# Kernel optimization log

Hardware: AMD Instinct MI355X
Metric: run time of the kernel (lower is better)

## Reference

```python
import jax, jax.numpy as jnp
import numpy as np


def _conv1x1(x, w, b=None):
    # x: [B,C,H,W], w: [O,C]
    y = jnp.einsum('bchw,oc->bohw', x, w)
    if b is not None:
        y = y + b[None, :, None, None]
    return y


def _conv3x3_dilated(x, w, b, dil):
    p = dil  # padding == dilation keeps spatial size for 3x3 kernels
    y = jax.lax.conv_general_dilated(
        x, w, window_strides=(1, 1), padding=((p, p), (p, p)),
        rhs_dilation=(dil, dil), dimension_numbers=('NCHW', 'OIHW', 'NCHW'))
    return y + b[None, :, None, None]


def _upsample2x_align_corners(x):
    # bilinear, align_corners=True, scale factor 2
    B, C, H, W = x.shape
    oh, ow = 2 * H, 2 * W
    ys = jnp.linspace(0.0, H - 1.0, oh)
    xs = jnp.linspace(0.0, W - 1.0, ow)
    y0 = jnp.floor(ys).astype(jnp.int32)
    x0 = jnp.floor(xs).astype(jnp.int32)
    y1 = jnp.minimum(y0 + 1, H - 1)
    x1 = jnp.minimum(x0 + 1, W - 1)
    wy = (ys - y0)[None, None, :, None]
    wx = (xs - x0)[None, None, None, :]
    gt = x[:, :, y0, :]
    gb = x[:, :, y1, :]
    top = gt[:, :, :, x0] * (1 - wx) + gt[:, :, :, x1] * wx
    bot = gb[:, :, :, x0] * (1 - wx) + gb[:, :, :, x1] * wx
    return top * (1 - wy) + bot * wy


def _gr(ftr, ck_w, ck_b, avg_w, max_w, gcn_w):
    # GR module: attention-diagonal graph conv with degree normalization
    B, C, H, W = ftr.shape
    HW = H * W
    # ChannelAttention_diag -> diagonal entries cw: [B, M]
    avg = ftr.mean(axis=(2, 3))
    mx = ftr.max(axis=(2, 3))
    cw = jax.nn.sigmoid(jax.nn.relu(avg @ avg_w.T) + jax.nn.relu(mx @ max_w.T))  # [B,M]
    k = jax.nn.relu(_conv1x1(ftr, ck_w, ck_b)).reshape(B, -1, HW)  # [B,M,HW]
    q = jnp.swapaxes(k, 1, 2)  # [B,HW,M]
    # A = sigmoid(q @ diag(cw) @ k); degree d = rowsum(A)^(-1/2)
    A = jax.nn.sigmoid(jnp.einsum('bim,bm,bmj->bij', q, cw, k))  # [B,HW,HW]
    d = A.sum(axis=2) ** -0.5  # [B,HW]
    P = d[:, :, None] * q  # D^{-1/2} @ q, [B,HW,M]
    X = jnp.swapaxes(ftr.reshape(B, C, HW), 1, 2)  # [B,HW,C]
    PtX = jnp.einsum('bjm,bjc->bmc', P, X)  # [B,M,C]
    LX = X - jnp.einsum('bim,bmc->bic', P, cw[:, :, None] * PtX)
    Y = X + LX @ gcn_w  # GCN (no bias)
    return jnp.swapaxes(Y, 1, 2).reshape(B, C, H, W)


def setup_inputs() -> dict:
    key = jax.random.key(0)
    ks = jax.random.split(key, 20)
    B, C = 64, 1024
    Cq = C // 4  # 256
    Mi = Cq // 2  # 128, ChannelAttention inter channels
    s = 0.02
    inp = {
        'x_cur': jax.random.normal(ks[0], (B, C, 16, 16), jnp.float32),
        'x_lat': jax.random.normal(ks[1], (B, C, 8, 8), jnp.float32),
        'conv_w': jax.random.normal(ks[2], (Cq, C), jnp.float32) * s,
        'conv_b': jax.random.normal(ks[3], (Cq,), jnp.float32) * s,
        'conv1_w': jax.random.normal(ks[4], (C, Cq), jnp.float32) * s,
        'conv1_b': jax.random.normal(ks[5], (C,), jnp.float32) * s,
        'conv3_w': jax.random.normal(ks[6], (C, 3 * Cq), jnp.float32) * s,
        'conv3_b': jax.random.normal(ks[7], (C,), jnp.float32) * s,
        'rate0_w': jax.random.normal(ks[8], (Cq, C, 3, 3), jnp.float32) * s,
        'rate0_b': jax.random.normal(ks[9], (Cq,), jnp.float32) * s,
        'rate1_w': jax.random.normal(ks[10], (Cq, C, 3, 3), jnp.float32) * s,
        'rate1_b': jax.random.normal(ks[11], (Cq,), jnp.float32) * s,
        'rate2_w': jax.random.normal(ks[12], (Cq, C, 3, 3), jnp.float32) * s,
        'rate2_b': jax.random.normal(ks[13], (Cq,), jnp.float32) * s,
        'gr_ck_w': jax.random.normal(ks[14], (Mi, Cq), jnp.float32) * s,
        'gr_ck_b': jax.random.normal(ks[15], (Mi,), jnp.float32) * s,
        'gr_avg_w': jax.random.normal(ks[16], (Mi, Cq), jnp.float32) * s,
        'gr_max_w': jax.random.normal(ks[17], (Mi, Cq), jnp.float32) * s,
        'gr_gcn_w': jax.random.normal(ks[18], (Cq, Cq), jnp.float32) * s,
        'pre': 1,
    }
    return inp


def reference(x_cur, x_lat, conv_w, conv_b, conv1_w, conv1_b, conv3_w, conv3_b,
              rate0_w, rate0_b, rate1_w, rate1_b, rate2_w, rate2_b,
              gr_ck_w, gr_ck_b, gr_avg_w, gr_max_w, gr_gcn_w, pre):
    # pre == 1 path of Graph_aspp.forward
    gr_args = (gr_ck_w, gr_ck_b, gr_avg_w, gr_max_w, gr_gcn_w)
    x_sum = x_cur * _upsample2x_align_corners(x_lat) + x_cur
    f1 = _conv3x3_dilated(x_sum, rate0_w, rate0_b, 1) + _conv1x1(x_sum, conv_w, conv_b)
    x1 = _gr(f1, *gr_args)
    feature = _conv1x1(f1, conv1_w, conv1_b) + x_sum
    f2 = _conv3x3_dilated(feature, rate1_w, rate1_b, 2) + _conv1x1(feature, conv_w, conv_b)
    x2 = _gr(f2, *gr_args)
    feature = _conv1x1(f2, conv1_w, conv1_b) + x_sum
    f3 = _conv3x3_dilated(feature, rate2_w, rate2_b, 4) + _conv1x1(feature, conv_w, conv_b)
    x3 = _gr(f3, *gr_args)
    cat = jnp.concatenate((x1, x2, x3), axis=1)
    return _conv1x1(cat, conv3_w, conv3_b)
```

## Files before the change

kernel.cpp:

```cpp
#include <hip/hip_runtime.h>

typedef unsigned short ushort_t;
typedef unsigned int uint32;
typedef __attribute__((ext_vector_type(8))) unsigned short ushort8;
typedef __attribute__((ext_vector_type(8))) __bf16 bf16x8;
typedef __attribute__((ext_vector_type(4))) float f32x4;

__device__ __forceinline__ ushort_t f2b(float f) {
    union { float f; uint32 u; } v; v.f = f;
    uint32 r = v.u + 0x7fffu + ((v.u >> 16) & 1u);
    return (ushort_t)(r >> 16);
}
__device__ __forceinline__ float b2f(ushort_t b) {
    union { uint32 u; float f; } v; v.u = ((uint32)b) << 16;
    return v.f;
}
__device__ __forceinline__ float sigm(float x) { return 1.f / (1.f + __expf(-x)); }

__device__ __forceinline__ void gload_lds16(const void* g, void* l) {
    __builtin_amdgcn_global_load_lds(
        (__attribute__((address_space(1))) void*)g,
        (__attribute__((address_space(3))) void*)l, 16, 0, 0);
}

constexpr int EPI_RELU  = 1;
constexpr int EPI_FEAT  = 2;
constexpr int EPI_SIG   = 3;
constexpr int EPI_XG    = 4;
constexpr int EPI_NEGCW = 5;
constexpr int EPI_Y     = 6;
constexpr int EPI_OUTT  = 7;

struct GemmP {
    const ushort_t* A; const ushort_t* B;
    const ushort_t* A2; const ushort_t* B2;
    long long aBatch, bBatch, a2Batch, b2Batch;
    int lda, ldb, lda2, ldb2;
    int Ksub, kSplit, dil;
    const float* bias;
    const ushort_t* res; long long resBatch; int ldres;
    ushort_t* obf; long long oBatch; int ldo;
    ushort_t* obf2;
    float* of32;
    const float* cw;
    float* dsum;
    const ushort_t* zpage;
};

__global__ __launch_bounds__(256) void gemm_big(GemmP p) {
    __shared__ __align__(16) ushort_t aT[128 * 64];
    __shared__ __align__(16) ushort_t bT[128 * 64];
    const int tid = threadIdx.x;
    const int z = blockIdx.z;
    const int m0 = blockIdx.x * 128, n0 = blockIdx.y * 128;
    const int lane = tid & 63, wid = tid >> 6;
    const int l15 = lane & 15, l16 = lane >> 4;
    const int wr = wid >> 1, wc = wid & 1;
    const int lrow = lane >> 3;
    const int sgran = (lane & 7) ^ lrow;

    int ayy[4], axx[4];
    const ushort_t* aBase[4];
    const ushort_t* bBase[4];
#pragma unroll
    for (int i = 0; i < 4; ++i) {
        int row = wid * 32 + i * 8 + lrow;
        int m = m0 + row;
        int bb = m >> 8;
        ayy[i] = (m >> 4) & 15; axx[i] = m & 15;
        aBase[i] = p.A + (long long)bb * 262144 + sgran * 8;
        bBase[i] = p.B + (long long)(n0 + row) * p.ldb + sgran * 8;
    }

    f32x4 acc[4][4];
#pragma unroll
    for (int i = 0; i < 4; ++i)
#pragma unroll
        for (int j = 0; j < 4; ++j) acc[i][j] = (f32x4){0.f, 0.f, 0.f, 0.f};

    const int gk0 = z * p.kSplit;
    const int iters = p.Ksub >> 6;
    for (int it = 0; it < iters; ++it) {
        const int gk = gk0 + it * 64;
        const int tap = gk >> 10, kin = gk & 1023;
        int dy = 0, dx = 0;
        if (tap < 9) { int ky = tap / 3; dy = (ky - 1) * p.dil; dx = (tap - ky * 3 - 1) * p.dil; }
#pragma unroll
        for (int i = 0; i < 4; ++i) {
            int iy = ayy[i] + dy, ix = axx[i] + dx;
            bool ok = ((unsigned)iy < 16u) && ((unsigned)ix < 16u);
            const ushort_t* ga = ok ? (aBase[i] + (((iy << 4) + ix) << 10) + kin) : p.zpage;
            gload_lds16(ga, &aT[(wid * 32 + i * 8) * 64]);
        }
#pragma unroll
        for (int i = 0; i < 4; ++i)
            gload_lds16(bBase[i] + gk, &bT[(wid * 32 + i * 8) * 64]);
        asm volatile("s_waitcnt vmcnt(0)" ::: "memory");
        __syncthreads();
#pragma unroll
        for (int ks = 0; ks < 2; ++ks) {
            bf16x8 af[4], bfr[4];
#pragma unroll
            for (int mi = 0; mi < 4; ++mi) {
                int rr = wr * 64 + mi * 16 + l15;
                int cc = (ks * 32 + l16 * 8) ^ ((rr & 7) << 3);
                af[mi] = __builtin_bit_cast(bf16x8, *(const ushort8*)&aT[rr * 64 + cc]);
            }
#pragma unroll
            for (int ni = 0; ni < 4; ++ni) {
                int rr = wc * 64 + ni * 16 + l15;
                int cc = (ks * 32 + l16 * 8) ^ ((rr & 7) << 3);
                bfr[ni] = __builtin_bit_cast(bf16x8, *(const ushort8*)&bT[rr * 64 + cc]);
            }
#pragma unroll
            for (int mi = 0; mi < 4; ++mi)
#pragma unroll
                for (int ni = 0; ni < 4; ++ni)
                    acc[mi][ni] = __builtin_amdgcn_mfma_f32_16x16x32_bf16(af[mi], bfr[ni], acc[mi][ni], 0, 0, 0);
        }
        __syncthreads();
    }
#pragma unroll
    for (int mi = 0; mi < 4; ++mi)
#pragma unroll
        for (int ni = 0; ni < 4; ++ni) {
            int gcol = n0 + wc * 64 + ni * 16 + l15;
            int growb = m0 + wr * 64 + mi * 16 + l16 * 4;
#pragma unroll
            for (int r = 0; r < 4; ++r)
                p.obf[(long long)z * p.oBatch + (long long)(growb + r) * 256 + gcol] =
                    f2b(acc[mi][ni][r]);
        }
}

template<int BM, int BN, int AMODE, int EPI>
__global__ __launch_bounds__(256) void gemm_k(GemmP p) {
    __shared__ __align__(16) ushort_t aT[BM * 64];
    __shared__ __align__(16) ushort_t bT[BN * 64];
    constexpr int APASS = BM / 32, BPASS = BN / 32;
    constexpr int MFRAG = BM / 32, NFRAG = BN / 32;
    const int tid = threadIdx.x;
    const int z = blockIdx.z;
    const int m0 = blockIdx.x * BM, n0 = blockIdx.y * BN;
    const int lane = tid & 63, wid = tid >> 6;
    const int l15 = lane & 15, l16 = lane >> 4;
    const int wr = wid >> 1, wc = wid & 1;
    const int srow = tid >> 3, scol = (tid & 7) * 8;
    const int swcol = scol ^ ((srow & 7) << 3);

    const ushort_t* aptr[APASS];
    const ushort_t* bptr[BPASS];
    const ushort_t* aptr2[APASS];
    const ushort_t* bptr2[BPASS];
#pragma unroll
    for (int pi = 0; pi < APASS; ++pi)
        aptr[pi] = p.A + (long long)z * p.aBatch +
                   (long long)(m0 + pi * 32 + srow) * p.lda + scol;
#pragma unroll
    for (int pi = 0; pi < BPASS; ++pi)
        bptr[pi] = p.B + (long long)z * p.bBatch +
                   (long long)(n0 + pi * 32 + srow) * p.ldb + scol;
    if constexpr (AMODE == 2) {
#pragma unroll
        for (int pi = 0; pi < APASS; ++pi)
            aptr2[pi] = p.A2 + (long long)z * p.a2Batch +
                        (long long)(m0 + pi * 32 + srow) * p.lda2 + scol;
#pragma unroll
        for (int pi = 0; pi < BPASS; ++pi)
            bptr2[pi] = p.B2 + (long long)z * p.b2Batch +
                        (long long)(n0 + pi * 32 + srow) * p.ldb2 + scol;
    }

    f32x4 acc[MFRAG][NFRAG];
#pragma unroll
    for (int i = 0; i < MFRAG; ++i)
#pragma unroll
        for (int j = 0; j < NFRAG; ++j) acc[i][j] = (f32x4){0.f, 0.f, 0.f, 0.f};

    ushort8 ar[APASS], br[BPASS];
    auto ldg = [&](int gk) {
        if (AMODE == 2 && gk >= 256) {
            int g2 = gk - 256;
#pragma unroll
            for (int pi = 0; pi < APASS; ++pi) ar[pi] = *(const ushort8*)(aptr2[pi] + g2);
#pragma unroll
            for (int pi = 0; pi < BPASS; ++pi) br[pi] = *(const ushort8*)(bptr2[pi] + g2);
        } else {
#pragma unroll
            for (int pi = 0; pi < APASS; ++pi) ar[pi] = *(const ushort8*)(aptr[pi] + gk);
#pragma unroll
            for (int pi = 0; pi < BPASS; ++pi) br[pi] = *(const ushort8*)(bptr[pi] + gk);
        }
    };

    const int gk0 = z * p.kSplit;
    ldg(gk0);
    const int iters = p.Ksub >> 6;
    for (int it = 0; it < iters; ++it) {
#pragma unroll
        for (int pi = 0; pi < APASS; ++pi)
            *(ushort8*)&aT[(pi * 32 + srow) * 64 + swcol] = ar[pi];
#pragma unroll
        for (int pi = 0; pi < BPASS; ++pi)
            *(ushort8*)&bT[(pi * 32 + srow) * 64 + swcol] = br[pi];
        __syncthreads();
        if (it + 1 < iters) ldg(gk0 + (it + 1) * 64);
#pragma unroll
        for (int ks = 0; ks < 2; ++ks) {
            bf16x8 af[MFRAG], bfr[NFRAG];
#pragma unroll
            for (int mi = 0; mi < MFRAG; ++mi) {
                int rr = wr * (BM / 2) + mi * 16 + l15;
                int cc = (ks * 32 + l16 * 8) ^ ((rr & 7) << 3);
                af[mi] = __builtin_bit_cast(bf16x8, *(const ushort8*)&aT[rr * 64 + cc]);
            }
#pragma unroll
            for (int ni = 0; ni < NFRAG; ++ni) {
                int rr = wc * (BN / 2) + ni * 16 + l15;
                int cc = (ks * 32 + l16 * 8) ^ ((rr & 7) << 3);
                bfr[ni] = __builtin_bit_cast(bf16x8, *(const ushort8*)&bT[rr * 64 + cc]);
            }
#pragma unroll
            for (int mi = 0; mi < MFRAG; ++mi)
#pragma unroll
                for (int ni = 0; ni < NFRAG; ++ni)
                    acc[mi][ni] = __builtin_amdgcn_mfma_f32_16x16x32_bf16(af[mi], bfr[ni], acc[mi][ni], 0, 0, 0);
        }
        __syncthreads();
    }

#pragma unroll
    for (int mi = 0; mi < MFRAG; ++mi) {
        if constexpr (EPI == EPI_SIG) {
#pragma unroll
            for (int r = 0; r < 4; ++r) {
                float sv = 0.f;
#pragma unroll
                for (int ni = 0; ni < NFRAG; ++ni) sv += sigm(acc[mi][ni][r]);
                sv += __shfl_xor(sv, 1); sv += __shfl_xor(sv, 2);
                sv += __shfl_xor(sv, 4); sv += __shfl_xor(sv, 8);
                if (l15 == 0) {
                    int grow = m0 + wr * (BM / 2) + mi * 16 + l16 * 4 + r;
                    int q4 = blockIdx.y * 2 + wc;
                    p.dsum[q4 * 16384 + z * 256 + grow] = sv;
                }
            }
        } else {
#pragma unroll
            for (int ni = 0; ni < NFRAG; ++ni) {
                int gcol = n0 + wc * (BN / 2) + ni * 16 + l15;
                int growb = m0 + wr * (BM / 2) + mi * 16 + l16 * 4;
#pragma unroll
                for (int r = 0; r < 4; ++r) {
                    int grow = growb + r;
                    float v = acc[mi][ni][r];
                    if constexpr (EPI == EPI_RELU) {
                        v += p.bias[gcol]; v = fmaxf(v, 0.f);
                        p.obf[(long long)grow * p.ldo + gcol] = f2b(v);
                        p.obf2[(long long)grow * p.ldo + gcol] =
                            f2b(v * p.cw[((grow >> 8) << 7) + gcol]);
                    } else if constexpr (EPI == EPI_FEAT) {
                        v += p.bias[gcol] + b2f(p.res[(long long)grow * p.ldres + gcol]);
                        p.obf[(long long)grow * p.ldo + gcol] = f2b(v);
                    } else if constexpr (EPI == EPI_XG) {
                        p.obf[(long long)z * p.oBatch + (long long)grow * p.ldo + gcol] = f2b(v);
                    } else if constexpr (EPI == EPI_NEGCW) {
                        v *= -p.cw[z * 128 + gcol];
                        p.obf[(long long)z * p.oBatch + (long long)grow * p.ldo + gcol] = f2b(v);
                    } else if constexpr (EPI == EPI_Y) {
                        v = b2f(p.res[(long long)z * p.resBatch + (long long)grow * p.ldres + gcol]) + v;
                        p.obf[(long long)z * p.oBatch + (long long)grow * p.ldo + gcol] = f2b(v);
                    } else if constexpr (EPI == EPI_OUTT) {
                        v += p.bias[grow];
                        int bb = gcol >> 8, px = gcol & 255;
                        p.of32[((long long)bb * 1024 + grow) * 256 + px] = v;
                    }
                }
            }
        }
    }
}


__global__ void k_combine(const ushort_t* __restrict__ t, const float* __restrict__ fbias_s,
                          ushort_t* __restrict__ f) {
    int idx = blockIdx.x * 256 + threadIdx.x;
    const long long N = 16384ll * 256;
    ushort8 a0 = *(const ushort8*)(t + (long long)idx * 8);
    ushort8 a1 = *(const ushort8*)(t + N + (long long)idx * 8);
    ushort8 a2 = *(const ushort8*)(t + 2 * N + (long long)idx * 8);
    ushort8 a3 = *(const ushort8*)(t + 3 * N + (long long)idx * 8);
    ushort8 a4 = *(const ushort8*)(t + 4 * N + (long long)idx * 8);
    int cb = (idx * 8) & 255;
    ushort8 o;
#pragma unroll
    for (int k = 0; k < 8; ++k)
        o[k] = f2b(b2f(a0[k]) + b2f(a1[k]) + b2f(a2[k]) + b2f(a3[k]) + b2f(a4[k]) + fbias_s[cb + k]);
    *(ushort8*)&f[(long long)idx * 8] = o;
}

__global__ void k_upsum(const float* __restrict__ xc, const float* __restrict__ xl,
                        ushort_t* __restrict__ xs) {
    __shared__ float lat[64 * 64];
    __shared__ ushort_t tile[64 * 258];
    int b = blockIdx.x, c0 = blockIdx.y * 64;
    int t = threadIdx.x;
    for (int i = t; i < 4096; i += 256)
        lat[i] = xl[((long long)(b * 1024 + c0 + (i >> 6))) * 64 + (i & 63)];
    __syncthreads();
    int y = t >> 4, x = t & 15;
    float fy = y * (7.f / 15.f); int y0 = (int)fy; float wy = fy - y0; int y1 = y0 + 1 > 7 ? 7 : y0 + 1;
    float fx = x * (7.f / 15.f); int x0 = (int)fx; float wx = fx - x0; int x1 = x0 + 1 > 7 ? 7 : x0 + 1;
    for (int cc = 0; cc < 64; ++cc) {
        float cur = xc[((long long)(b * 1024 + c0 + cc)) * 256 + t];
        const float* L = &lat[cc * 64];
        float tv = L[y0 * 8 + x0] * (1.f - wx) + L[y0 * 8 + x1] * wx;
        float bv = L[y1 * 8 + x0] * (1.f - wx) + L[y1 * 8 + x1] * wx;
        float up = tv + (bv - tv) * wy;
        tile[cc * 258 + t] = f2b(cur * (1.f + up));
    }
    __syncthreads();
    for (int i = t; i < 16384; i += 256) {
        int px = i >> 6, cc = i & 63;
        xs[((long long)(b * 256 + px)) * 1024 + c0 + cc] = tile[cc * 258 + px];
    }
}

__global__ void k_poolcw(const ushort_t* __restrict__ f,
                         const float* __restrict__ aw, const float* __restrict__ mw,
                         float* __restrict__ cw) {
    __shared__ float sa[256], sm[256];
    int b = blockIdx.x, t = threadIdx.x;
    float s = 0.f, m = -3.4e38f;
    const ushort_t* base = f + (long long)b * 65536 + t;
    for (int px = 0; px < 256; ++px) { float v = b2f(base[px * 256]); s += v; m = fmaxf(m, v); }
    sa[t] = s * (1.f / 256.f);
    sm[t] = m;
    __syncthreads();
    if (t < 128) {
        float s1 = 0.f, s2 = 0.f;
        const float* a = aw + t * 256; const float* w = mw + t * 256;
        for (int c = 0; c < 256; ++c) { s1 += sa[c] * a[c]; s2 += sm[c] * w[c]; }
        s1 = fmaxf(s1, 0.f); s2 = fmaxf(s2, 0.f);
        cw[b * 128 + t] = sigm(s1 + s2);
    }
}

__global__ void k_pscale(const ushort_t* __restrict__ q, const float* __restrict__ dsum4,
                         ushort_t* __restrict__ P, ushort_t* __restrict__ Pt) {
    __shared__ ushort_t t[128][130];
    __shared__ float dd[128];
    int jh = blockIdx.x, b = blockIdx.y;
    int j0 = jh * 128;
    int tid = threadIdx.x;
    if (tid < 128) {
        int pix = b * 256 + j0 + tid;
        float s = dsum4[pix] + dsum4[16384 + pix] + dsum4[32768 + pix] + dsum4[49152 + pix];
        dd[tid] = rsqrtf(s);
    }
    __syncthreads();
    int jr = tid >> 7, m = tid & 127;
    for (int i = 0; i < 64; ++i) {
        int j = i * 2 + jr;
        long long qi = ((long long)(b * 256 + j0 + j)) * 128 + m;
        ushort_t v = f2b(dd[j] * b2f(q[qi]));
        P[qi] = v;
        t[j][m] = v;
    }
    __syncthreads();
    for (int i = 0; i < 64; ++i) {
        int mm = i * 2 + jr;
        Pt[((long long)b << 15) + (mm << 8) + j0 + m] = t[m][mm];
    }
}

__global__ void k_packall(const float* r0, const float* r1, const float* r2,
                          const float* convw, const float* c1w, const float* c3w,
                          const float* ckw, const float* gcnw,
                          const float* rb0, const float* rb1, const float* rb2,
                          const float* cb,
                          ushort_t* wbig3, ushort_t* w1b, ushort_t* w3b,
                          ushort_t* ckb, ushort_t* gcnT, float* fbias,
                          ushort_t* zpage) {
    int blk = blockIdx.x, tid = threadIdx.x;
    if (blk < 768) {
        __shared__ float lw[10240];
        int s = blk >> 8, o = blk & 255;
        const float* rate = s == 0 ? r0 : (s == 1 ? r1 : r2);
        for (int i = tid; i < 9216; i += 256) lw[i] = rate[(long long)o * 9216 + i];
        for (int i = tid; i < 1024; i += 256) lw[9216 + i] = convw[(long long)o * 1024 + i];
        __syncthreads();
        ushort_t* dst = wbig3 + (long long)blk * 10240;
        for (int i = tid; i < 10240; i += 256) {
            int tap = i >> 10, ci = i & 1023;
            float v = (tap < 9) ? lw[ci * 9 + tap] : lw[9216 + i - 9216 + ci - ci];
            v = (tap < 9) ? lw[ci * 9 + tap] : lw[9216 + ci];
            dst[i] = f2b(v);
        }
        return;
    }
    const int R1 = 262144, R2 = R1 + 786432, R3 = R2 + 32768, R4 = R3 + 65536;
    const int R5 = R4 + 768, R6 = R5 + 128;
    int base = (blk - 768) * 2048 + tid * 8;
#pragma unroll
    for (int k = 0; k < 8; ++k) {
        int i = base + k;
        if (i >= R6) return;
        if (i < R1) w1b[i] = f2b(c1w[i]);
        else if (i < R2) w3b[i - R1] = f2b(c3w[i - R1]);
        else if (i < R3) ckb[i - R2] = f2b(ckw[i - R2]);
        else if (i < R4) {
            int ii = i - R3; int c2 = ii >> 8, c1 = ii & 255;
            gcnT[ii] = f2b(gcnw[c1 * 256 + c2]);
        } else if (i < R5) {
            int ii = i - R4; int s = ii >> 8, t = ii & 255;
            const float* rb = s == 0 ? rb0 : (s == 1 ? rb1 : rb2);
            fbias[ii] = rb[t] + cb[t];
        } else {
            zpage[i - R5] = 0;
        }
    }
}

__global__ void k_sentinel(float* o, int n, float v) {
    int i = blockIdx.x * 256 + threadIdx.x; if (i < n) o[i] = v;
}

extern "C" void kernel_launch(void* const* d_in, const int* in_sizes, int n_in,
                              void* d_out, int out_size, void* d_ws, size_t ws_size,
                              hipStream_t stream) {
    const float* x_cur  = (const float*)d_in[0];
    const float* x_lat  = (const float*)d_in[1];
    const float* conv_w = (const float*)d_in[2];
    const float* conv_b = (const float*)d_in[3];
    const float* conv1_w = (const float*)d_in[4];
    const float* conv1_b = (const float*)d_in[5];
    const float* conv3_w = (const float*)d_in[6];
    const float* conv3_b = (const float*)d_in[7];
    const float* rate_w[3] = {(const float*)d_in[8], (const float*)d_in[10], (const float*)d_in[12]};
    const float* rate_b[3] = {(const float*)d_in[9], (const float*)d_in[11], (const float*)d_in[13]};
    const float* ck_w  = (const float*)d_in[14];
    const float* ck_b  = (const float*)d_in[15];
    const float* avg_w = (const float*)d_in[16];
    const float* max_w = (const float*)d_in[17];
    const float* gcn_w = (const float*)d_in[18];
    float* out = (float*)d_out;

    char* w = (char*)d_ws;
    auto take = [&](size_t bytes) { void* p = (void*)w; w += (bytes + 255) & ~(size_t)255; return p; };
    ushort_t* xsum  = (ushort_t*)take(16384ll * 1024 * 2);
    ushort_t* feat  = (ushort_t*)take(16384ll * 1024 * 2);
    ushort_t* fbuf  = (ushort_t*)take(16384ll * 256 * 2);
    ushort_t* xgt   = (ushort_t*)take(64ll * 256 * 256 * 2);
    ushort_t* qbuf  = (ushort_t*)take(16384ll * 128 * 2);
    ushort_t* qc    = (ushort_t*)take(16384ll * 128 * 2);
    ushort_t* Pt    = (ushort_t*)take(64ll * 128 * 256 * 2);
    ushort_t* Pb    = (ushort_t*)take(16384ll * 128 * 2);
    ushort_t* Htn   = (ushort_t*)take(64ll * 256 * 128 * 2);
    ushort_t* wbig3 = (ushort_t*)take(3ll * 256 * 10240 * 2);
    ushort_t* w1b   = (ushort_t*)take(1024ll * 256 * 2);
    ushort_t* w3b   = (ushort_t*)take(1024ll * 768 * 2);
    ushort_t* ckb   = (ushort_t*)take(128ll * 256 * 2);
    ushort_t* gcnT  = (ushort_t*)take(256ll * 256 * 2);
    ushort_t* zpage = (ushort_t*)take(256);
    float*    fbias = (float*)take(3 * 256 * 4);
    float*    cwb   = (float*)take(64 * 128 * 4);
    float*    dsum4 = (float*)take(4ll * 64 * 256 * 4);
    ushort_t* catb  = (ushort_t*)take(16384ll * 768 * 2);
    ushort_t* ftmp  = (ushort_t*)take(5ll * 16384 * 256 * 2);
    size_t need = (size_t)(w - (char*)d_ws);

    if (need > ws_size) {
        float v = 1.0e6f + (float)(ws_size >> 20);
        k_sentinel<<<(out_size + 255) / 256, 256, 0, stream>>>(out, out_size, v);
        return;
    }

    k_packall<<<768 + 561, 256, 0, stream>>>(
        rate_w[0], rate_w[1], rate_w[2], conv_w, conv1_w, conv3_w, ck_w, gcn_w,
        rate_b[0], rate_b[1], rate_b[2], conv_b,
        wbig3, w1b, w3b, ckb, gcnT, fbias, zpage);
    k_upsum<<<dim3(64, 16), 256, 0, stream>>>(x_cur, x_lat, xsum);

    for (int s = 0; s < 3; ++s) {
        {
            GemmP p{};
            p.A = (s == 0) ? xsum : feat;
            p.B = wbig3 + (long long)s * 256 * 10240; p.ldb = 10240;
            p.Ksub = 2048; p.kSplit = 2048; p.dil = 1 << s;
            p.obf = ftmp; p.oBatch = 16384ll * 256;
            p.zpage = zpage;
            gemm_big<<<dim3(128, 2, 5), 256, 0, stream>>>(p);
        }
        k_combine<<<2048, 256, 0, stream>>>(ftmp, fbias + s * 256, fbuf);
        k_poolcw<<<64, 256, 0, stream>>>(fbuf, avg_w, max_w, cwb);
        {
            GemmP p{};
            p.A = fbuf; p.lda = 256; p.B = ckb; p.ldb = 256;
            p.Ksub = 256;
            p.bias = ck_b; p.obf = qbuf; p.obf2 = qc; p.cw = cwb; p.ldo = 128;
            gemm_k<128, 128, 0, EPI_RELU><<<dim3(128, 1, 1), 256, 0, stream>>>(p);
        }
        {
            GemmP p{};
            p.A = qc;   p.aBatch = 32768; p.lda = 128;
            p.B = qbuf; p.bBatch = 32768; p.ldb = 128;
            p.Ksub = 128; p.dsum = dsum4;
            gemm_k<128, 128, 0, EPI_SIG><<<dim3(2, 2, 64), 256, 0, stream>>>(p);
        }
        k_pscale<<<dim3(2, 64), 256, 0, stream>>>(qbuf, dsum4, Pb, Pt);
        {
            GemmP p{};
            p.A = gcnT; p.aBatch = 0;     p.lda = 256;
            p.B = fbuf; p.bBatch = 65536; p.ldb = 256;
            p.Ksub = 256;
            p.obf = xgt; p.oBatch = 65536; p.ldo = 256;
            gemm_k<128, 128, 0, EPI_XG><<<dim3(2, 2, 64), 256, 0, stream>>>(p);
        }
        {
            GemmP p{};
            p.A = xgt; p.aBatch = 65536; p.lda = 256;
            p.B = Pt;  p.bBatch = 32768; p.ldb = 256;
            p.Ksub = 256; p.cw = cwb;
            p.obf = Htn; p.oBatch = 32768; p.ldo = 128;
            gemm_k<128, 128, 0, EPI_NEGCW><<<dim3(2, 1, 64), 256, 0, stream>>>(p);
        }
        {
            GemmP p{};
            p.A = fbuf; p.aBatch = 65536; p.lda = 256;
            p.B = gcnT; p.bBatch = 0;     p.ldb = 256;
            p.A2 = Pb;  p.a2Batch = 32768; p.lda2 = 128;
            p.B2 = Htn; p.b2Batch = 32768; p.ldb2 = 128;
            p.Ksub = 384;
            p.res = fbuf; p.resBatch = 65536; p.ldres = 256;
            p.obf = catb + s * 256; p.oBatch = 256ll * 768; p.ldo = 768;
            gemm_k<128, 128, 2, EPI_Y><<<dim3(2, 2, 64), 256, 0, stream>>>(p);
        }
        if (s < 2) {
            GemmP p{};
            p.A = fbuf; p.lda = 256; p.B = w1b; p.ldb = 256;
            p.Ksub = 256; p.bias = conv1_b;
            p.res = xsum; p.ldres = 1024;
            p.obf = feat; p.ldo = 1024;
            gemm_k<128, 128, 0, EPI_FEAT><<<dim3(128, 8, 1), 256, 0, stream>>>(p);
        }
    }
    {
        GemmP p{};
        p.A = w3b;  p.lda = 768;
        p.B = catb; p.ldb = 768;
        p.Ksub = 768; p.bias = conv3_b; p.of32 = out;
        gemm_k<128, 128, 0, EPI_OUTT><<<dim3(8, 128, 1), 256, 0, stream>>>(p);
    }
}
```

Baseline: 762.1 us.

## Use 64x64 tiles for small GR GEMMs and fold cw scaling into A-load

Switches the graph-reasoning GEMMs (ck conv, attention/sigmoid degree sum, XG, NEGCW, Y, conv1 feature) from 128x128 to 64x64 tiles with proportionally larger grids, so these small batched GEMMs launch more blocks and fill more compute units. The cw-scaled copy of q is no longer written by the ReLU epilogue. Instead a new A-load mode multiplies A by cw while loading, which removes one buffer write and read. The degree partial sums grow from 4 to 8 slices to match the finer column split. The tradeoff is less operand reuse per tile and an extra multiply-and-round on every A element load.

```diff
diff --git a/kernel.cpp b/kernel.cpp
--- a/kernel.cpp
+++ b/kernel.cpp
@@ -40,7 +40,6 @@
     const float* bias;
     const ushort_t* res; long long resBatch; int ldres;
     ushort_t* obf; long long oBatch; int ldo;
-    ushort_t* obf2;
     float* of32;
     const float* cw;
     float* dsum;
@@ -185,6 +184,17 @@
             for (int pi = 0; pi < APASS; ++pi) ar[pi] = *(const ushort8*)(aptr2[pi] + g2);
 #pragma unroll
             for (int pi = 0; pi < BPASS; ++pi) br[pi] = *(const ushort8*)(bptr2[pi] + g2);
+        } else if constexpr (AMODE == 3) {
+#pragma unroll
+            for (int pi = 0; pi < APASS; ++pi) {
+                ushort8 t8 = *(const ushort8*)(aptr[pi] + gk);
+#pragma unroll
+                for (int k = 0; k < 8; ++k)
+                    t8[k] = f2b(b2f(t8[k]) * p.cw[(z << 7) + gk + scol + k]);
+                ar[pi] = t8;
+            }
+#pragma unroll
+            for (int pi = 0; pi < BPASS; ++pi) br[pi] = *(const ushort8*)(bptr[pi] + gk);
         } else {
 #pragma unroll
             for (int pi = 0; pi < APASS; ++pi) ar[pi] = *(const ushort8*)(aptr[pi] + gk);
@@ -241,8 +251,8 @@
                 sv += __shfl_xor(sv, 4); sv += __shfl_xor(sv, 8);
                 if (l15 == 0) {
                     int grow = m0 + wr * (BM / 2) + mi * 16 + l16 * 4 + r;
-                    int q4 = blockIdx.y * 2 + wc;
-                    p.dsum[q4 * 16384 + z * 256 + grow] = sv;
+                    int q8 = blockIdx.y * 2 + wc;
+                    p.dsum[q8 * 16384 + z * 256 + grow] = sv;
                 }
             }
         } else {
@@ -257,8 +267,6 @@
                     if constexpr (EPI == EPI_RELU) {
                         v += p.bias[gcol]; v = fmaxf(v, 0.f);
                         p.obf[(long long)grow * p.ldo + gcol] = f2b(v);
-                        p.obf2[(long long)grow * p.ldo + gcol] =
-                            f2b(v * p.cw[((grow >> 8) << 7) + gcol]);
                     } else if constexpr (EPI == EPI_FEAT) {
                         v += p.bias[gcol] + b2f(p.res[(long long)grow * p.ldres + gcol]);
                         p.obf[(long long)grow * p.ldo + gcol] = f2b(v);
@@ -346,7 +354,7 @@
     }
 }
 
-__global__ void k_pscale(const ushort_t* __restrict__ q, const float* __restrict__ dsum4,
+__global__ void k_pscale(const ushort_t* __restrict__ q, const float* __restrict__ dsum8,
                          ushort_t* __restrict__ P, ushort_t* __restrict__ Pt) {
     __shared__ ushort_t t[128][130];
     __shared__ float dd[128];
@@ -355,7 +363,9 @@
     int tid = threadIdx.x;
     if (tid < 128) {
         int pix = b * 256 + j0 + tid;
-        float s = dsum4[pix] + dsum4[16384 + pix] + dsum4[32768 + pix] + dsum4[49152 + pix];
+        float s = 0.f;
+#pragma unroll
+        for (int qs = 0; qs < 8; ++qs) s += dsum8[qs * 16384 + pix];
         dd[tid] = rsqrtf(s);
     }
     __syncthreads();
@@ -393,8 +403,7 @@
         ushort_t* dst = wbig3 + (long long)blk * 10240;
         for (int i = tid; i < 10240; i += 256) {
             int tap = i >> 10, ci = i & 1023;
-            float v = (tap < 9) ? lw[ci * 9 + tap] : lw[9216 + i - 9216 + ci - ci];
-            v = (tap < 9) ? lw[ci * 9 + tap] : lw[9216 + ci];
+            float v = (tap < 9) ? lw[ci * 9 + tap] : lw[9216 + ci];
             dst[i] = f2b(v);
         }
         return;
@@ -453,7 +462,6 @@
     ushort_t* fbuf  = (ushort_t*)take(16384ll * 256 * 2);
     ushort_t* xgt   = (ushort_t*)take(64ll * 256 * 256 * 2);
     ushort_t* qbuf  = (ushort_t*)take(16384ll * 128 * 2);
-    ushort_t* qc    = (ushort_t*)take(16384ll * 128 * 2);
     ushort_t* Pt    = (ushort_t*)take(64ll * 128 * 256 * 2);
     ushort_t* Pb    = (ushort_t*)take(16384ll * 128 * 2);
     ushort_t* Htn   = (ushort_t*)take(64ll * 256 * 128 * 2);
@@ -465,7 +473,7 @@
     ushort_t* zpage = (ushort_t*)take(256);
     float*    fbias = (float*)take(3 * 256 * 4);
     float*    cwb   = (float*)take(64 * 128 * 4);
-    float*    dsum4 = (float*)take(4ll * 64 * 256 * 4);
+    float*    dsum8 = (float*)take(8ll * 64 * 256 * 4);
     ushort_t* catb  = (ushort_t*)take(16384ll * 768 * 2);
     ushort_t* ftmp  = (ushort_t*)take(5ll * 16384 * 256 * 2);
     size_t need = (size_t)(w - (char*)d_ws);
@@ -498,24 +506,24 @@
             GemmP p{};
             p.A = fbuf; p.lda = 256; p.B = ckb; p.ldb = 256;
             p.Ksub = 256;
-            p.bias = ck_b; p.obf = qbuf; p.obf2 = qc; p.cw = cwb; p.ldo = 128;
-            gemm_k<128, 128, 0, EPI_RELU><<<dim3(128, 1, 1), 256, 0, stream>>>(p);
+            p.bias = ck_b; p.obf = qbuf; p.ldo = 128;
+            gemm_k<64, 64, 0, EPI_RELU><<<dim3(256, 2, 1), 256, 0, stream>>>(p);
         }
         {
             GemmP p{};
-            p.A = qc;   p.aBatch = 32768; p.lda = 128;
+            p.A = qbuf; p.aBatch = 32768; p.lda = 128;
             p.B = qbuf; p.bBatch = 32768; p.ldb = 128;
-            p.Ksub = 128; p.dsum = dsum4;
-            gemm_k<128, 128, 0, EPI_SIG><<<dim3(2, 2, 64), 256, 0, stream>>>(p);
-        }
-        k_pscale<<<dim3(2, 64), 256, 0, stream>>>(qbuf, dsum4, Pb, Pt);
+            p.Ksub = 128; p.dsum = dsum8; p.cw = cwb;
+            gemm_k<64, 64, 3, EPI_SIG><<<dim3(4, 4, 64), 256, 0, stream>>>(p);
+        }
+        k_pscale<<<dim3(2, 64), 256, 0, stream>>>(qbuf, dsum8, Pb, Pt);
         {
             GemmP p{};
             p.A = gcnT; p.aBatch = 0;     p.lda = 256;
             p.B = fbuf; p.bBatch = 65536; p.ldb = 256;
             p.Ksub = 256;
             p.obf = xgt; p.oBatch = 65536; p.ldo = 256;
-            gemm_k<128, 128, 0, EPI_XG><<<dim3(2, 2, 64), 256, 0, stream>>>(p);
+            gemm_k<64, 64, 0, EPI_XG><<<dim3(4, 4, 64), 256, 0, stream>>>(p);
         }
         {
             GemmP p{};
@@ -523,7 +531,7 @@
             p.B = Pt;  p.bBatch = 32768; p.ldb = 256;
             p.Ksub = 256; p.cw = cwb;
             p.obf = Htn; p.oBatch = 32768; p.ldo = 128;
-            gemm_k<128, 128, 0, EPI_NEGCW><<<dim3(2, 1, 64), 256, 0, stream>>>(p);
+            gemm_k<64, 64, 0, EPI_NEGCW><<<dim3(4, 2, 64), 256, 0, stream>>>(p);
         }
         {
             GemmP p{};
@@ -534,7 +542,7 @@
             p.Ksub = 384;
             p.res = fbuf; p.resBatch = 65536; p.ldres = 256;
             p.obf = catb + s * 256; p.oBatch = 256ll * 768; p.ldo = 768;
-            gemm_k<128, 128, 2, EPI_Y><<<dim3(2, 2, 64), 256, 0, stream>>>(p);
+            gemm_k<64, 64, 2, EPI_Y><<<dim3(4, 4, 64), 256, 0, stream>>>(p);
         }
         if (s < 2) {
             GemmP p{};
@@ -542,7 +550,7 @@
             p.Ksub = 256; p.bias = conv1_b;
             p.res = xsum; p.ldres = 1024;
             p.obf = feat; p.ldo = 1024;
-            gemm_k<128, 128, 0, EPI_FEAT><<<dim3(128, 8, 1), 256, 0, stream>>>(p);
+            gemm_k<64, 64, 0, EPI_FEAT><<<dim3(256, 16, 1), 256, 0, stream>>>(p);
         }
     }
     {
```

New measurement: 696.1 us. 8.7% less time.
